# Optimization experiments

Hardware: AMD Instinct MI355X
Metric: run time of the kernel (lower is better)

## Reference

```python
import jax, jax.numpy as jnp
import numpy as np

B, C, IMG, P = 64, 3, 224, 16
GRID = IMG // P          # 14
N = GRID * GRID          # 196 patch tokens
D = 768
L, H = 12, 12
HD = D // H              # 64
FF = 4 * D               # 3072
NC = 1000
PRUNE_LAYER = 6
KEEP = max(1, int(N * 0.5))  # 98 tokens kept after pruning
LN_EPS = 1e-6


def _ln(x, g, b):
    m = jnp.mean(x, axis=-1, keepdims=True)
    v = jnp.var(x, axis=-1, keepdims=True)
    return (x - m) * jax.lax.rsqrt(v + LN_EPS) * g + b


def _block(x, g1, b1, qw, qb, pw, pb, g2, b2, w1, c1, w2, c2):
    # standard timm ViT block: x + Attn(LN(x)); x + MLP(LN(x))
    Bq, S, _ = x.shape
    h = _ln(x, g1, b1)
    qkv = (h @ qw + qb).reshape(Bq, S, 3, H, HD)
    q, k, v = qkv[:, :, 0], qkv[:, :, 1], qkv[:, :, 2]  # [B,S,H,HD]
    attn = jax.nn.softmax(jnp.einsum('bqhd,bkhd->bhqk', q, k) * (HD ** -0.5), axis=-1)
    o = jnp.einsum('bhqk,bkhd->bqhd', attn, v).reshape(Bq, S, D)
    x = x + o @ pw + pb
    h = _ln(x, g2, b2)
    return x + jax.nn.gelu(h @ w1 + c1, approximate=False) @ w2 + c2


def _forward(x, patch_w, patch_b, cls_token, pos_embed, ln1_g, ln1_b, qkv_w, qkv_b,
             proj_w, proj_b, ln2_g, ln2_b, fc1_w, fc1_b, fc2_w, fc2_b,
             norm_g, norm_b, head_w, head_b):
    Bq = x.shape[0]
    # patch embed: conv(k=16, s=16) == patchify + linear; flatten order (C, ph, pw) matches torch conv weight layout
    patches = x.reshape(Bq, C, GRID, P, GRID, P).transpose(0, 2, 4, 1, 3, 5).reshape(Bq, N, C * P * P)
    t = patches @ patch_w + patch_b                                     # [B,N,D]
    t = jnp.concatenate([jnp.broadcast_to(cls_token, (Bq, 1, D)), t], axis=1) + pos_embed  # [B,197,D]

    blk = lambda t, i: _block(t, ln1_g[i], ln1_b[i], qkv_w[i], qkv_b[i], proj_w[i], proj_b[i],
                              ln2_g[i], ln2_b[i], fc1_w[i], fc1_b[i], fc2_w[i], fc2_b[i])
    for i in range(PRUNE_LAYER):
        t = blk(t, i)

    cls_tok, patch_tok = t[:, :1], t[:, 1:]
    # per-token L2 scores + topk selection + gather (the irregular-access stage)
    scores = jnp.sqrt(jnp.sum(patch_tok * patch_tok, axis=-1))          # [B,N]
    _, idx = jax.lax.top_k(scores, KEEP)                                # sorted descending, matches torch.topk
    sel = jnp.take_along_axis(patch_tok, idx[:, :, None], axis=1)       # [B,K,D]
    t = jnp.concatenate([cls_tok, sel], axis=1)                         # [B,K+1,D]

    for i in range(PRUNE_LAYER, L):
        t = blk(t, i)
    t = _ln(t, norm_g, norm_b)
    return t[:, 0] @ head_w + head_b                                    # [B,NC]


def setup_inputs() -> dict:
    key = jax.random.key(0)
    ks = jax.random.split(key, 12)
    s = 0.02
    f32 = jnp.float32
    return {
        'x': jax.random.normal(ks[0], (B, C, IMG, IMG), f32),
        'patch_w': jax.random.normal(ks[1], (C * P * P, D), f32) * s,
        'patch_b': jnp.zeros((D,), f32),
        'cls_token': jax.random.normal(ks[2], (1, 1, D), f32) * s,
        'pos_embed': jax.random.normal(ks[3], (1, N + 1, D), f32) * s,
        'ln1_g': jnp.ones((L, D), f32), 'ln1_b': jnp.zeros((L, D), f32),
        'qkv_w': jax.random.normal(ks[4], (L, D, 3 * D), f32) * s,
        'qkv_b': jnp.zeros((L, 3 * D), f32),
        'proj_w': jax.random.normal(ks[5], (L, D, D), f32) * s,
        'proj_b': jnp.zeros((L, D), f32),
        'ln2_g': jnp.ones((L, D), f32), 'ln2_b': jnp.zeros((L, D), f32),
        'fc1_w': jax.random.normal(ks[6], (L, D, FF), f32) * s,
        'fc1_b': jnp.zeros((L, FF), f32),
        'fc2_w': jax.random.normal(ks[7], (L, FF, D), f32) * s,
        'fc2_b': jnp.zeros((L, D), f32),
        'norm_g': jnp.ones((D,), f32), 'norm_b': jnp.zeros((D,), f32),
        'head_w': jax.random.normal(ks[8], (D, NC), f32) * s,
        'head_b': jnp.zeros((NC,), f32),
    }


def reference(x, patch_w, patch_b, cls_token, pos_embed, ln1_g, ln1_b, qkv_w, qkv_b,
              proj_w, proj_b, ln2_g, ln2_b, fc1_w, fc1_b, fc2_w, fc2_b,
              norm_g, norm_b, head_w, head_b):
    return _forward(x, patch_w, patch_b, cls_token, pos_embed, ln1_g, ln1_b, qkv_w, qkv_b,
                    proj_w, proj_b, ln2_g, ln2_b, fc1_w, fc1_b, fc2_w, fc2_b,
                    norm_g, norm_b, head_w, head_b)
```

## Files before the change

### kernel.cpp

```cpp
#include <hip/hip_runtime.h>
#include <hip/hip_bf16.h>
#include <cstddef>
#include <cstdint>

namespace {

constexpr int B = 64, CIN = 3, IMG = 224, PS = 16, GRID_ = 14, NPATCH = 196;
constexpr int D = 768, H = 12, HD = 64, FFD = 3072, NC = 1000;
constexpr int S1 = 197, S2 = 99, KEEP = 98, PRUNE = 6, LAYERS = 12;
constexpr float LN_EPS = 1e-6f;

typedef __attribute__((ext_vector_type(8))) short bf16x8;
typedef __attribute__((ext_vector_type(4))) float f32x4;

__device__ inline float wave_red_sum(float v) {
  #pragma unroll
  for (int off = 32; off > 0; off >>= 1) v += __shfl_xor(v, off, 64);
  return v;
}

__device__ inline void gl16(const __hip_bfloat16* g, __hip_bfloat16* l) {
  __builtin_amdgcn_global_load_lds(
      (const __attribute__((address_space(1))) void*)g,
      (__attribute__((address_space(3))) void*)l,
      16, 0, 0);
}

__global__ __launch_bounds__(256) void tcvt_k(const float* __restrict__ src,
                                              __hip_bfloat16* __restrict__ dst,
                                              int R, int C, size_t lstride) {
  src += (size_t)blockIdx.z * lstride;
  dst += (size_t)blockIdx.z * lstride;
  __shared__ float tile[32][33];
  int c0 = blockIdx.x * 32, r0 = blockIdx.y * 32;
  int tx = threadIdx.x & 31, ty = threadIdx.x >> 5;
  #pragma unroll
  for (int i = 0; i < 32; i += 8) {
    int r = r0 + ty + i, c = c0 + tx;
    tile[ty + i][tx] = (r < R && c < C) ? src[(size_t)r * C + c] : 0.f;
  }
  __syncthreads();
  #pragma unroll
  for (int i = 0; i < 32; i += 8) {
    int c = c0 + ty + i, r = r0 + tx;
    if (c < C && r < R) dst[(size_t)c * R + r] = __float2bfloat16(tile[tx][ty + i]);
  }
}

__global__ void patchify_k(const float* __restrict__ x, __hip_bfloat16* __restrict__ out) {
  size_t idx = (size_t)blockIdx.x * blockDim.x + threadIdx.x;
  size_t total = (size_t)B * NPATCH * D;
  if (idx >= total) return;
  int row = (int)(idx / D), k = (int)(idx % D);
  int b = row / NPATCH, n = row % NPATCH;
  int gr = n / GRID_, gc = n % GRID_;
  int c = k / (PS * PS), rr = (k % (PS * PS)) / PS, cc = k % PS;
  out[idx] = __float2bfloat16(x[((size_t)(b * CIN + c) * IMG + (gr * PS + rr)) * IMG + gc * PS + cc]);
}

template <int MODE>
__global__ __launch_bounds__(256) void bgemm_k(
    const __hip_bfloat16* __restrict__ A, const __hip_bfloat16* __restrict__ BT,
    const float* __restrict__ bias, void* __restrict__ Cc,
    int M, int N, int K, const float* __restrict__ extra) {
  __shared__ __hip_bfloat16 As[3][128 * 32];
  __shared__ __hip_bfloat16 Bs[3][128 * 32];
  int tid = threadIdx.x, lane = tid & 63, wv = tid >> 6;
  int wr = wv >> 1, wc = wv & 1;
  int m0 = blockIdx.y * 128, n0 = blockIdx.x * 128;
  int fr = lane & 15, fq = lane >> 4;
  int srow = lane >> 2;
  int scd = (lane & 3) ^ ((lane >> 3) & 3);
  int rswz = (fq ^ ((fr >> 1) & 3)) * 8;
  int nk = K >> 5;

  auto stage = [&](int buf, int kt) {
    int k0 = kt << 5;
    #pragma unroll
    for (int i = 0; i < 2; ++i) {
      int r = wv * 32 + i * 16 + srow;
      int gra = m0 + r; gra = (gra < M) ? gra : (M - 1);
      gl16(A + (size_t)gra * K + k0 + scd * 8, &As[buf][(wv * 32 + i * 16) * 32]);
      int grb = n0 + r; grb = (grb < N) ? grb : (N - 1);
      gl16(BT + (size_t)grb * K + k0 + scd * 8, &Bs[buf][(wv * 32 + i * 16) * 32]);
    }
  };

  f32x4 acc[4][4] = {};
  stage(0, 0);
  if (nk > 1) stage(1, 1);
  for (int kt = 0; kt < nk; ++kt) {
    int buf = kt % 3;
    if (kt + 2 < nk) {
      stage((kt + 2) % 3, kt + 2);
      asm volatile("s_waitcnt vmcnt(8)" ::: "memory");
    } else if (kt + 1 < nk) {
      asm volatile("s_waitcnt vmcnt(4)" ::: "memory");
    } else {
      asm volatile("s_waitcnt vmcnt(0)" ::: "memory");
    }
    asm volatile("s_barrier" ::: "memory");
    bf16x8 af[4], bg[4];
    #pragma unroll
    for (int m = 0; m < 4; ++m)
      af[m] = *(const bf16x8*)&As[buf][(wr * 64 + m * 16 + fr) * 32 + rswz];
    #pragma unroll
    for (int n = 0; n < 4; ++n)
      bg[n] = *(const bf16x8*)&Bs[buf][(wc * 64 + n * 16 + fr) * 32 + rswz];
    #pragma unroll
    for (int m = 0; m < 4; ++m)
      #pragma unroll
      for (int n = 0; n < 4; ++n)
        acc[m][n] = __builtin_amdgcn_mfma_f32_16x16x32_bf16(af[m], bg[n], acc[m][n], 0, 0, 0);
    asm volatile("s_waitcnt lgkmcnt(0)" ::: "memory");
    asm volatile("s_barrier" ::: "memory");
  }
  #pragma unroll
  for (int m = 0; m < 4; ++m) {
    #pragma unroll
    for (int n = 0; n < 4; ++n) {
      #pragma unroll
      for (int j = 0; j < 4; ++j) {
        int row = m0 + wr * 64 + m * 16 + fq * 4 + j;
        int col = n0 + wc * 64 + n * 16 + fr;
        if (row >= M || col >= N) continue;
        float v = acc[m][n][j] + bias[col];
        if (MODE == 0) {
          ((__hip_bfloat16*)Cc)[(size_t)row * N + col] = __float2bfloat16(v);
        } else if (MODE == 1) {
          int b = row / NPATCH, nn = row % NPATCH;
          ((float*)Cc)[((size_t)(b * S1 + 1 + nn)) * D + col] = v + extra[(size_t)(1 + nn) * D + col];
        } else if (MODE == 2) {
          ((float*)Cc)[(size_t)row * N + col] += v;
        } else {
          float g = 0.5f * v * (1.0f + erff(v * 0.7071067811865476f));
          ((__hip_bfloat16*)Cc)[(size_t)row * N + col] = __float2bfloat16(g);
        }
      }
    }
  }
}

__global__ __launch_bounds__(256) void gemm_k(
    const float* __restrict__ A, const float* __restrict__ Bw,
    const float* __restrict__ bias, float* __restrict__ Cc,
    int M, int N, int K) {
  __shared__ float As[64][17];
  __shared__ float Bs[16][64];
  int tid = threadIdx.x;
  int tx = tid & 15, ty = tid >> 4;
  int m0 = blockIdx.y * 64, n0 = blockIdx.x * 64;
  float acc[4][4] = {};
  for (int k0 = 0; k0 < K; k0 += 16) {
    #pragma unroll
    for (int j = 0; j < 4; ++j) {
      int i = tid + 256 * j;
      int r = i >> 4, c = i & 15;
      int gr = m0 + r;
      As[r][c] = (gr < M) ? A[(size_t)gr * K + (k0 + c)] : 0.f;
    }
    #pragma unroll
    for (int j = 0; j < 4; ++j) {
      int i = tid + 256 * j;
      int r = i >> 6, c = i & 63;
      int gc = n0 + c;
      Bs[r][c] = (gc < N) ? Bw[(size_t)(k0 + r) * N + gc] : 0.f;
    }
    __syncthreads();
    #pragma unroll
    for (int kk = 0; kk < 16; ++kk) {
      float a[4], bb[4];
      #pragma unroll
      for (int ii = 0; ii < 4; ++ii) a[ii] = As[ty * 4 + ii][kk];
      #pragma unroll
      for (int jj = 0; jj < 4; ++jj) bb[jj] = Bs[kk][tx * 4 + jj];
      #pragma unroll
      for (int ii = 0; ii < 4; ++ii)
        #pragma unroll
        for (int jj = 0; jj < 4; ++jj) acc[ii][jj] = fmaf(a[ii], bb[jj], acc[ii][jj]);
    }
    __syncthreads();
  }
  #pragma unroll
  for (int ii = 0; ii < 4; ++ii) {
    int row = m0 + ty * 4 + ii;
    if (row >= M) continue;
    #pragma unroll
    for (int jj = 0; jj < 4; ++jj) {
      int col = n0 + tx * 4 + jj;
      if (col >= N) continue;
      Cc[(size_t)row * N + col] = acc[ii][jj] + bias[col];
    }
  }
}

__global__ void cls_init_k(float* __restrict__ t, const float* __restrict__ cls,
                           const float* __restrict__ pos) {
  int idx = blockIdx.x * blockDim.x + threadIdx.x;
  if (idx >= B * D) return;
  int b = idx / D, d = idx % D;
  t[(size_t)b * S1 * D + d] = cls[d] + pos[d];
}

template <typename OutT>
__global__ __launch_bounds__(256) void ln_k(const float* __restrict__ in, OutT* __restrict__ out,
                                            const float* __restrict__ g, const float* __restrict__ bta,
                                            size_t istride, size_t ostride) {
  int row = blockIdx.x;
  const float* p = in + (size_t)row * istride;
  int tid = threadIdx.x;
  float v0 = p[tid], v1 = p[tid + 256], v2 = p[tid + 512];
  float s = v0 + v1 + v2;
  float s2 = v0 * v0 + v1 * v1 + v2 * v2;
  s = wave_red_sum(s);
  s2 = wave_red_sum(s2);
  __shared__ float r1[4], r2[4];
  int lane = tid & 63, w = tid >> 6;
  if (lane == 0) { r1[w] = s; r2[w] = s2; }
  __syncthreads();
  s = r1[0] + r1[1] + r1[2] + r1[3];
  s2 = r2[0] + r2[1] + r2[2] + r2[3];
  float mean = s * (1.0f / 768.0f);
  float var = s2 * (1.0f / 768.0f) - mean * mean;
  float rs = rsqrtf(var + LN_EPS);
  OutT* q = out + (size_t)row * ostride;
  #pragma unroll
  for (int c = 0; c < 3; ++c) {
    int i = tid + 256 * c;
    float vv = (c == 0 ? v0 : (c == 1 ? v1 : v2));
    float r = (vv - mean) * rs * g[i] + bta[i];
    if constexpr (sizeof(OutT) == 2) q[i] = __float2bfloat16(r);
    else q[i] = r;
  }
}

template <int NT16>
__global__ __launch_bounds__(256) void attn3_k(const __hip_bfloat16* __restrict__ qkv,
                                               __hip_bfloat16* __restrict__ o, int S) {
  constexpr int NT32 = (NT16 + 1) / 2;
  constexpr int COLS = NT32 * 32;
  constexpr int STR = COLS + 8;
  __shared__ __hip_bfloat16 VT[64 * STR];
  __shared__ __hip_bfloat16 P[4][16 * STR];
  int bh = blockIdx.x;
  int b = bh / H, hh = bh % H;
  int tid = threadIdx.x, lane = tid & 63, wv = tid >> 6;
  int fr = lane & 15, fq = lane >> 4;
  const size_t rs = 3 * D;
  const __hip_bfloat16* qb = qkv + ((size_t)b * S) * rs + hh * HD;
  const __hip_bfloat16* kb = qb + D;
  const __hip_bfloat16* vb = qb + 2 * D;
  const __hip_bfloat16 z = __float2bfloat16(0.f);
  for (int idx = tid; idx < COLS * 64; idx += 256) {
    int key = idx >> 6, d = idx & 63;
    VT[d * STR + key] = (key < S) ? vb[(size_t)key * rs + d] : z;
  }
  if (NT16 & 1) {
    for (int idx = lane; idx < 16 * 16; idx += 64)
      P[wv][(idx >> 4) * STR + NT16 * 16 + (idx & 15)] = z;
  }
  __syncthreads();

  for (int qt = wv; qt * 16 < S; qt += 4) {
    int q0 = qt * 16;
    int qrow = q0 + fr;
    const __hip_bfloat16* qp = qb + (size_t)(qrow < S ? qrow : 0) * rs + fq * 8;
    bf16x8 aq0 = *(const bf16x8*)(qp);
    bf16x8 aq1 = *(const bf16x8*)(qp + 32);
    f32x4 sc[NT16];
    #pragma unroll
    for (int kt = 0; kt < NT16; ++kt) {
      int krow = kt * 16 + fr;
      const __hip_bfloat16* kp = kb + (size_t)(krow < S ? krow : 0) * rs + fq * 8;
      bf16x8 bk0 = *(const bf16x8*)(kp);
      bf16x8 bk1 = *(const bf16x8*)(kp + 32);
      f32x4 a = {};
      a = __builtin_amdgcn_mfma_f32_16x16x32_bf16(aq0, bk0, a, 0, 0, 0);
      a = __builtin_amdgcn_mfma_f32_16x16x32_bf16(aq1, bk1, a, 0, 0, 0);
      sc[kt] = a;
    }
    float lj[4];
    #pragma unroll
    for (int jj = 0; jj < 4; ++jj) {
      float mx = -1e30f;
      #pragma unroll
      for (int kt = 0; kt < NT16; ++kt) {
        float v = sc[kt][jj] * 0.125f;
        if (kt * 16 + fr >= S) v = -1e30f;
        sc[kt][jj] = v;
        mx = fmaxf(mx, v);
      }
      mx = fmaxf(mx, __shfl_xor(mx, 1, 64));
      mx = fmaxf(mx, __shfl_xor(mx, 2, 64));
      mx = fmaxf(mx, __shfl_xor(mx, 4, 64));
      mx = fmaxf(mx, __shfl_xor(mx, 8, 64));
      float sum = 0.f;
      #pragma unroll
      for (int kt = 0; kt < NT16; ++kt) {
        float p = __expf(sc[kt][jj] - mx);
        sc[kt][jj] = p;
        sum += p;
      }
      sum += __shfl_xor(sum, 1, 64);
      sum += __shfl_xor(sum, 2, 64);
      sum += __shfl_xor(sum, 4, 64);
      sum += __shfl_xor(sum, 8, 64);
      lj[jj] = 1.0f / sum;
    }
    __hip_bfloat16* pw = &P[wv][0];
    #pragma unroll
    for (int kt = 0; kt < NT16; ++kt)
      #pragma unroll
      for (int jj = 0; jj < 4; ++jj)
        pw[(fq * 4 + jj) * STR + kt * 16 + fr] = __float2bfloat16(sc[kt][jj]);
    #pragma unroll
    for (int dt = 0; dt < 4; ++dt) {
      f32x4 oa = {};
      #pragma unroll
      for (int kc = 0; kc < NT32; ++kc) {
        bf16x8 ap = *(const bf16x8*)&pw[fr * STR + kc * 32 + fq * 8];
        bf16x8 bv = *(const bf16x8*)&VT[(dt * 16 + fr) * STR + kc * 32 + fq * 8];
        oa = __builtin_amdgcn_mfma_f32_16x16x32_bf16(ap, bv, oa, 0, 0, 0);
      }
      #pragma unroll
      for (int jj = 0; jj < 4; ++jj) {
        int orow = q0 + fq * 4 + jj;
        if (orow < S)
          o[((size_t)(b * S + orow)) * D + hh * HD + dt * 16 + fr] =
              __float2bfloat16(oa[jj] * lj[jj]);
      }
    }
  }
}

__global__ void score_k(const float* __restrict__ t, float* __restrict__ scores) {
  int gw = (blockIdx.x * blockDim.x + threadIdx.x) >> 6;
  int lane = threadIdx.x & 63;
  if (gw >= B * NPATCH) return;
  int b = gw / NPATCH, n = gw % NPATCH;
  const float* p = t + ((size_t)(b * S1) + 1 + n) * D;
  float a = 0.f;
  #pragma unroll
  for (int j = lane; j < D; j += 64) { float v = p[j]; a += v * v; }
  a = wave_red_sum(a);
  if (lane == 0) scores[gw] = sqrtf(a);
}

__global__ __launch_bounds__(256) void select_k(const float* __restrict__ scores, int* __restrict__ map) {
  int b = blockIdx.x;
  __shared__ float s[NPATCH];
  __shared__ int flag[NPATCH];
  int i = threadIdx.x;
  if (i < NPATCH) s[i] = scores[b * NPATCH + i];
  __syncthreads();
  if (i < NPATCH) {
    float si = s[i];
    int r = 0;
    for (int j = 0; j < NPATCH; ++j) {
      float sj = s[j];
      r += (sj > si) || (sj == si && j < i);
    }
    flag[i] = (r < KEEP) ? 1 : 0;
  }
  __syncthreads();
  if (i < NPATCH && flag[i]) {
    int p = 0;
    for (int j = 0; j < i; ++j) p += flag[j];
    map[b * (KEEP + 1) + 1 + p] = 1 + i;
  }
  if (i == 0) map[b * (KEEP + 1)] = 0;
}

__global__ void gather_k(const float* __restrict__ t, const int* __restrict__ map,
                         float* __restrict__ t2) {
  int br = blockIdx.x;
  int b = br / S2;
  int src = map[br];
  const float* p = t + ((size_t)b * S1 + src) * D;
  float* q = t2 + (size_t)br * D;
  for (int j = threadIdx.x; j < D; j += blockDim.x) q[j] = p[j];
}

}

extern "C" void kernel_launch(void* const* d_in, const int* in_sizes, int n_in,
                              void* d_out, int out_size, void* d_ws, size_t ws_size,
                              hipStream_t stream) {
  const float* x       = (const float*)d_in[0];
  const float* patch_w = (const float*)d_in[1];
  const float* patch_b = (const float*)d_in[2];
  const float* cls_tok = (const float*)d_in[3];
  const float* pos_emb = (const float*)d_in[4];
  const float* ln1_g   = (const float*)d_in[5];
  const float* ln1_b   = (const float*)d_in[6];
  const float* qkv_w   = (const float*)d_in[7];
  const float* qkv_b   = (const float*)d_in[8];
  const float* proj_w  = (const float*)d_in[9];
  const float* proj_b  = (const float*)d_in[10];
  const float* ln2_g   = (const float*)d_in[11];
  const float* ln2_b   = (const float*)d_in[12];
  const float* fc1_w   = (const float*)d_in[13];
  const float* fc1_b   = (const float*)d_in[14];
  const float* fc2_w   = (const float*)d_in[15];
  const float* fc2_b   = (const float*)d_in[16];
  const float* norm_g  = (const float*)d_in[17];
  const float* norm_b  = (const float*)d_in[18];
  const float* head_w  = (const float*)d_in[19];
  const float* head_b  = (const float*)d_in[20];
  float* out = (float*)d_out;

  char* wp = (char*)d_ws;
  auto alloc = [&](size_t bytes) { char* r = wp; wp += (bytes + 255) & ~(size_t)255; return r; };
  float* t   = (float*)alloc((size_t)B * S1 * D * 4);
  float* t2  = (float*)alloc((size_t)B * S2 * D * 4);
  float* hf  = (float*)alloc((size_t)B * D * 4);
  float* scores = (float*)alloc((size_t)B * NPATCH * 4);
  int*   map    = (int*)alloc((size_t)B * S2 * 4);
  __hip_bfloat16* h   = (__hip_bfloat16*)alloc((size_t)B * S1 * D * 2);
  __hip_bfloat16* qkv = (__hip_bfloat16*)alloc((size_t)B * S1 * 3 * D * 2);
  __hip_bfloat16* ff  = (__hip_bfloat16*)alloc((size_t)B * S1 * FFD * 2);
  __hip_bfloat16* qkvT  = (__hip_bfloat16*)alloc((size_t)LAYERS * 3 * D * D * 2);
  __hip_bfloat16* projT = (__hip_bfloat16*)alloc((size_t)LAYERS * D * D * 2);
  __hip_bfloat16* fc1T  = (__hip_bfloat16*)alloc((size_t)LAYERS * FFD * D * 2);
  __hip_bfloat16* fc2T  = (__hip_bfloat16*)alloc((size_t)LAYERS * D * FFD * 2);
  __hip_bfloat16* patchT = (__hip_bfloat16*)alloc((size_t)D * D * 2);
  __hip_bfloat16* patches = ff;

  { dim3 g(3 * D / 32, D / 32, LAYERS);
    tcvt_k<<<g, 256, 0, stream>>>(qkv_w, qkvT, D, 3 * D, (size_t)D * 3 * D); }
  { dim3 g(D / 32, D / 32, LAYERS);
    tcvt_k<<<g, 256, 0, stream>>>(proj_w, projT, D, D, (size_t)D * D); }
  { dim3 g(FFD / 32, D / 32, LAYERS);
    tcvt_k<<<g, 256, 0, stream>>>(fc1_w, fc1T, D, FFD, (size_t)D * FFD); }
  { dim3 g(D / 32, FFD / 32, LAYERS);
    tcvt_k<<<g, 256, 0, stream>>>(fc2_w, fc2T, FFD, D, (size_t)FFD * D); }
  { dim3 g(D / 32, D / 32, 1);
    tcvt_k<<<g, 256, 0, stream>>>(patch_w, patchT, D, D, 0); }

  {
    size_t total = (size_t)B * NPATCH * D;
    patchify_k<<<(unsigned)((total + 255) / 256), 256, 0, stream>>>(x, patches);
    dim3 g(D / 128, (B * NPATCH) / 128);
    bgemm_k<1><<<g, 256, 0, stream>>>(patches, patchT, patch_b, t, B * NPATCH, D, D, pos_emb);
    cls_init_k<<<(B * D + 255) / 256, 256, 0, stream>>>(t, cls_tok, pos_emb);
  }

  auto run_block = [&](float* tb, int S, int l) {
    int M = B * S;
    int mb = (M + 127) / 128;
    ln_k<__hip_bfloat16><<<M, 256, 0, stream>>>(tb, h, ln1_g + (size_t)l * D, ln1_b + (size_t)l * D, D, D);
    { dim3 g(3 * D / 128, mb);
      bgemm_k<0><<<g, 256, 0, stream>>>(h, qkvT + (size_t)l * 3 * D * D, qkv_b + (size_t)l * 3 * D,
                                        qkv, M, 3 * D, D, nullptr); }
    if (S == S1) attn3_k<13><<<B * H, 256, 0, stream>>>(qkv, h, S);
    else         attn3_k<7><<<B * H, 256, 0, stream>>>(qkv, h, S);
    { dim3 g(D / 128, mb);
      bgemm_k<2><<<g, 256, 0, stream>>>(h, projT + (size_t)l * D * D, proj_b + (size_t)l * D,
                                        tb, M, D, D, nullptr); }
    ln_k<__hip_bfloat16><<<M, 256, 0, stream>>>(tb, h, ln2_g + (size_t)l * D, ln2_b + (size_t)l * D, D, D);
    { dim3 g(FFD / 128, mb);
      bgemm_k<3><<<g, 256, 0, stream>>>(h, fc1T + (size_t)l * FFD * D, fc1_b + (size_t)l * FFD,
                                        ff, M, FFD, D, nullptr); }
    { dim3 g(D / 128, mb);
      bgemm_k<2><<<g, 256, 0, stream>>>(ff, fc2T + (size_t)l * D * FFD, fc2_b + (size_t)l * D,
                                        tb, M, D, FFD, nullptr); }
  };

  for (int l = 0; l < PRUNE; ++l) run_block(t, S1, l);

  score_k<<<(B * NPATCH * 64 + 255) / 256, 256, 0, stream>>>(t, scores);
  select_k<<<B, 256, 0, stream>>>(scores, map);
  gather_k<<<B * S2, 256, 0, stream>>>(t, map, t2);

  for (int l = PRUNE; l < LAYERS; ++l) run_block(t2, S2, l);

  ln_k<float><<<B, 256, 0, stream>>>(t2, hf, norm_g, norm_b, (size_t)S2 * D, D);
  { dim3 g((NC + 63) / 64, (B + 63) / 64);
    gemm_k<<<g, 256, 0, stream>>>(hf, head_w, head_b, out, B, NC, D); }
}
```

Measured before the change: 5.011 ms.

## Add XCD-aware grouped tile remap, compile-time K in GEMM, vectorize layernorm

The GEMM kernel now remaps its flat block index so that consecutive blocks on each of the 8 XCDs cover grouped column-major super-tiles of 8 row tiles. The aim is better L2 reuse of A and B tiles within an XCD. K becomes a template parameter with precomputed row pointers and a partially unrolled k-loop, which cuts address arithmetic. LayerNorm switches to 192 threads, each with one float4 load and vectorized stores, reducing instruction count; this assumes 16-byte aligned rows.

```diff
diff --git a/kernel.cpp b/kernel.cpp
--- a/kernel.cpp
+++ b/kernel.cpp
@@ -58,43 +58,71 @@
   out[idx] = __float2bfloat16(x[((size_t)(b * CIN + c) * IMG + (gr * PS + rr)) * IMG + gc * PS + cc]);
 }
 
-template <int MODE>
+template <int MODE, int KC>
 __global__ __launch_bounds__(256) void bgemm_k(
     const __hip_bfloat16* __restrict__ A, const __hip_bfloat16* __restrict__ BT,
     const float* __restrict__ bias, void* __restrict__ Cc,
-    int M, int N, int K, const float* __restrict__ extra) {
+    int M, int N, const float* __restrict__ extra) {
   __shared__ __hip_bfloat16 As[3][128 * 32];
   __shared__ __hip_bfloat16 Bs[3][128 * 32];
   int tid = threadIdx.x, lane = tid & 63, wv = tid >> 6;
   int wr = wv >> 1, wc = wv & 1;
-  int m0 = blockIdx.y * 128, n0 = blockIdx.x * 128;
+
+  int nbx = gridDim.x, nby = gridDim.y;
+  int nwg = nbx * nby;
+  int flat = blockIdx.y * nbx + blockIdx.x;
+  int q8 = nwg >> 3, r8 = nwg & 7;
+  int xcd = flat & 7, pos = flat >> 3;
+  int nf = (xcd < r8 ? xcd * (q8 + 1) : r8 * (q8 + 1) + (xcd - r8) * q8) + pos;
+  constexpr int G = 8;
+  int fullS = nby / G, tailR = nby - fullS * G;
+  int fullCount = fullS * G * nbx;
+  int bx, by;
+  if (nf < fullCount) {
+    int sup = nf / (G * nbx);
+    int rem = nf - sup * G * nbx;
+    bx = rem / G;
+    by = sup * G + (rem - bx * G);
+  } else {
+    int rem = nf - fullCount;
+    bx = rem / tailR;
+    by = fullS * G + (rem - bx * tailR);
+  }
+  int m0 = by * 128, n0 = bx * 128;
+
   int fr = lane & 15, fq = lane >> 4;
   int srow = lane >> 2;
   int scd = (lane & 3) ^ ((lane >> 3) & 3);
   int rswz = (fq ^ ((fr >> 1) & 3)) * 8;
-  int nk = K >> 5;
+  constexpr int NK = KC >> 5;
+
+  int r0i = m0 + wv * 32 + srow, r1i = r0i + 16;
+  int ga0 = (r0i < M) ? r0i : (M - 1), ga1 = (r1i < M) ? r1i : (M - 1);
+  int c0i = n0 + wv * 32 + srow, c1i = c0i + 16;
+  int gb0 = (c0i < N) ? c0i : (N - 1), gb1 = (c1i < N) ? c1i : (N - 1);
+  const __hip_bfloat16* pa0 = A + (size_t)ga0 * KC + scd * 8;
+  const __hip_bfloat16* pa1 = A + (size_t)ga1 * KC + scd * 8;
+  const __hip_bfloat16* pb0 = BT + (size_t)gb0 * KC + scd * 8;
+  const __hip_bfloat16* pb1 = BT + (size_t)gb1 * KC + scd * 8;
 
   auto stage = [&](int buf, int kt) {
-    int k0 = kt << 5;
-    #pragma unroll
-    for (int i = 0; i < 2; ++i) {
-      int r = wv * 32 + i * 16 + srow;
-      int gra = m0 + r; gra = (gra < M) ? gra : (M - 1);
-      gl16(A + (size_t)gra * K + k0 + scd * 8, &As[buf][(wv * 32 + i * 16) * 32]);
-      int grb = n0 + r; grb = (grb < N) ? grb : (N - 1);
-      gl16(BT + (size_t)grb * K + k0 + scd * 8, &Bs[buf][(wv * 32 + i * 16) * 32]);
-    }
+    int ko = kt << 5;
+    gl16(pa0 + ko, &As[buf][(wv * 32) * 32]);
+    gl16(pa1 + ko, &As[buf][(wv * 32 + 16) * 32]);
+    gl16(pb0 + ko, &Bs[buf][(wv * 32) * 32]);
+    gl16(pb1 + ko, &Bs[buf][(wv * 32 + 16) * 32]);
   };
 
   f32x4 acc[4][4] = {};
   stage(0, 0);
-  if (nk > 1) stage(1, 1);
-  for (int kt = 0; kt < nk; ++kt) {
+  stage(1, 1);
+  #pragma unroll 4
+  for (int kt = 0; kt < NK; ++kt) {
     int buf = kt % 3;
-    if (kt + 2 < nk) {
+    if (kt + 2 < NK) {
       stage((kt + 2) % 3, kt + 2);
       asm volatile("s_waitcnt vmcnt(8)" ::: "memory");
-    } else if (kt + 1 < nk) {
+    } else if (kt + 1 < NK) {
       asm volatile("s_waitcnt vmcnt(4)" ::: "memory");
     } else {
       asm volatile("s_waitcnt vmcnt(0)" ::: "memory");
@@ -203,34 +231,37 @@
 }
 
 template <typename OutT>
-__global__ __launch_bounds__(256) void ln_k(const float* __restrict__ in, OutT* __restrict__ out,
+__global__ __launch_bounds__(192) void ln_k(const float* __restrict__ in, OutT* __restrict__ out,
                                             const float* __restrict__ g, const float* __restrict__ bta,
                                             size_t istride, size_t ostride) {
-  int row = blockIdx.x;
-  const float* p = in + (size_t)row * istride;
-  int tid = threadIdx.x;
-  float v0 = p[tid], v1 = p[tid + 256], v2 = p[tid + 512];
-  float s = v0 + v1 + v2;
-  float s2 = v0 * v0 + v1 * v1 + v2 * v2;
+  int row = blockIdx.x, tid = threadIdx.x;
+  const float4* p = (const float4*)(in + (size_t)row * istride);
+  float4 v = p[tid];
+  float s = v.x + v.y + v.z + v.w;
+  float s2 = v.x * v.x + v.y * v.y + v.z * v.z + v.w * v.w;
   s = wave_red_sum(s);
   s2 = wave_red_sum(s2);
-  __shared__ float r1[4], r2[4];
+  __shared__ float r1[3], r2[3];
   int lane = tid & 63, w = tid >> 6;
   if (lane == 0) { r1[w] = s; r2[w] = s2; }
   __syncthreads();
-  s = r1[0] + r1[1] + r1[2] + r1[3];
-  s2 = r2[0] + r2[1] + r2[2] + r2[3];
+  s = r1[0] + r1[1] + r1[2];
+  s2 = r2[0] + r2[1] + r2[2];
   float mean = s * (1.0f / 768.0f);
   float var = s2 * (1.0f / 768.0f) - mean * mean;
   float rs = rsqrtf(var + LN_EPS);
-  OutT* q = out + (size_t)row * ostride;
-  #pragma unroll
-  for (int c = 0; c < 3; ++c) {
-    int i = tid + 256 * c;
-    float vv = (c == 0 ? v0 : (c == 1 ? v1 : v2));
-    float r = (vv - mean) * rs * g[i] + bta[i];
-    if constexpr (sizeof(OutT) == 2) q[i] = __float2bfloat16(r);
-    else q[i] = r;
+  float4 gv = ((const float4*)g)[tid];
+  float4 bv = ((const float4*)bta)[tid];
+  float o0 = (v.x - mean) * rs * gv.x + bv.x;
+  float o1 = (v.y - mean) * rs * gv.y + bv.y;
+  float o2 = (v.z - mean) * rs * gv.z + bv.z;
+  float o3 = (v.w - mean) * rs * gv.w + bv.w;
+  if constexpr (sizeof(OutT) == 2) {
+    __hip_bfloat16 hb[4] = {__float2bfloat16(o0), __float2bfloat16(o1),
+                            __float2bfloat16(o2), __float2bfloat16(o3)};
+    *(uint2*)((__hip_bfloat16*)out + (size_t)row * ostride + tid * 4) = *(uint2*)hb;
+  } else {
+    ((float4*)((float*)out + (size_t)row * ostride))[tid] = make_float4(o0, o1, o2, o3);
   }
 }
 
@@ -441,29 +472,29 @@
     size_t total = (size_t)B * NPATCH * D;
     patchify_k<<<(unsigned)((total + 255) / 256), 256, 0, stream>>>(x, patches);
     dim3 g(D / 128, (B * NPATCH) / 128);
-    bgemm_k<1><<<g, 256, 0, stream>>>(patches, patchT, patch_b, t, B * NPATCH, D, D, pos_emb);
+    bgemm_k<1, 768><<<g, 256, 0, stream>>>(patches, patchT, patch_b, t, B * NPATCH, D, pos_emb);
     cls_init_k<<<(B * D + 255) / 256, 256, 0, stream>>>(t, cls_tok, pos_emb);
   }
 
   auto run_block = [&](float* tb, int S, int l) {
     int M = B * S;
     int mb = (M + 127) / 128;
-    ln_k<__hip_bfloat16><<<M, 256, 0, stream>>>(tb, h, ln1_g + (size_t)l * D, ln1_b + (size_t)l * D, D, D);
+    ln_k<__hip_bfloat16><<<M, 192, 0, stream>>>(tb, h, ln1_g + (size_t)l * D, ln1_b + (size_t)l * D, D, D);
     { dim3 g(3 * D / 128, mb);
-      bgemm_k<0><<<g, 256, 0, stream>>>(h, qkvT + (size_t)l * 3 * D * D, qkv_b + (size_t)l * 3 * D,
-                                        qkv, M, 3 * D, D, nullptr); }
+      bgemm_k<0, 768><<<g, 256, 0, stream>>>(h, qkvT + (size_t)l * 3 * D * D, qkv_b + (size_t)l * 3 * D,
+                                             qkv, M, 3 * D, nullptr); }
     if (S == S1) attn3_k<13><<<B * H, 256, 0, stream>>>(qkv, h, S);
     else         attn3_k<7><<<B * H, 256, 0, stream>>>(qkv, h, S);
     { dim3 g(D / 128, mb);
-      bgemm_k<2><<<g, 256, 0, stream>>>(h, projT + (size_t)l * D * D, proj_b + (size_t)l * D,
-                                        tb, M, D, D, nullptr); }
-    ln_k<__hip_bfloat16><<<M, 256, 0, stream>>>(tb, h, ln2_g + (size_t)l * D, ln2_b + (size_t)l * D, D, D);
+      bgemm_k<2, 768><<<g, 256, 0, stream>>>(h, projT + (size_t)l * D * D, proj_b + (size_t)l * D,
+                                             tb, M, D, nullptr); }
+    ln_k<__hip_bfloat16><<<M, 192, 0, stream>>>(tb, h, ln2_g + (size_t)l * D, ln2_b + (size_t)l * D, D, D);
     { dim3 g(FFD / 128, mb);
-      bgemm_k<3><<<g, 256, 0, stream>>>(h, fc1T + (size_t)l * FFD * D, fc1_b + (size_t)l * FFD,
-                                        ff, M, FFD, D, nullptr); }
+      bgemm_k<3, 768><<<g, 256, 0, stream>>>(h, fc1T + (size_t)l * FFD * D, fc1_b + (size_t)l * FFD,
+                                             ff, M, FFD, nullptr); }
     { dim3 g(D / 128, mb);
-      bgemm_k<2><<<g, 256, 0, stream>>>(ff, fc2T + (size_t)l * D * FFD, fc2_b + (size_t)l * D,
-                                        tb, M, D, FFD, nullptr); }
+      bgemm_k<2, 3072><<<g, 256, 0, stream>>>(ff, fc2T + (size_t)l * D * FFD, fc2_b + (size_t)l * D,
+                                              tb, M, D, nullptr); }
   };
 
   for (int l = 0; l < PRUNE; ++l) run_block(t, S1, l);
@@ -474,7 +505,7 @@
 
   for (int l = PRUNE; l < LAYERS; ++l) run_block(t2, S2, l);
 
-  ln_k<float><<<B, 256, 0, stream>>>(t2, hf, norm_g, norm_b, (size_t)S2 * D, D);
+  ln_k<float><<<B, 192, 0, stream>>>(t2, hf, norm_g, norm_b, (size_t)S2 * D, D);
   { dim3 g((NC + 63) / 64, (B + 63) / 64);
     gemm_k<<<g, 256, 0, stream>>>(hf, head_w, head_b, out, B, NC, D); }
 }
```

Result: slower. 5.778 ms (+15.3%).
